# Kernel optimization log

Hardware: AMD Instinct MI355X
Metric: run time of the kernel (lower is better)

## Reference

```python
import jax, jax.numpy as jnp
import numpy as np

OMEGA_ENC = 0.01   # Encoder.omega
OMEGA_K = 0.1      # KernelMLP.omega
N0, E0 = 4096, 16384     # level-0 graph
N1, E1 = 1024, 8192      # level-1 (pooled) graph
F_IN, H, LAT, DIM = 8, 64, 32, 3
F = H + DIM              # conv input features (x || pos)


def _glorot(key, shape):
    s = jnp.sqrt(2.0 / (shape[0] + shape[-1]))
    return (jax.random.normal(key, shape) * s).astype(jnp.float32)


def setup_inputs() -> dict:
    key = jax.random.key(0)
    ks = jax.random.split(key, 24)
    inp = {
        "x": jax.random.normal(ks[0], (N0, F_IN), jnp.float32),
        "pos": jax.random.normal(ks[1], (N0, DIM), jnp.float32),
        "edge_index": jax.random.randint(ks[2], (2, E0), 0, N0),
        "pool_edge_index1": jax.random.randint(ks[3], (2, E1), 0, N1),
        "pool_pos1": jax.random.normal(ks[4], (N1, DIM), jnp.float32),
        "pool_keep_idx0": jnp.sort(jax.random.randint(ks[5], (N1,), 0, N0)),
        "lin0_w": _glorot(ks[6], (F_IN, H)),
        "lin0_b": 0.01 * jax.random.normal(ks[7], (H,), jnp.float32),
        "lin1_w": _glorot(ks[8], (H, LAT)),
        "lin1_b": 0.01 * jax.random.normal(ks[9], (LAT,), jnp.float32),
    }
    k = 10
    for i in range(2):
        inp[f"conv{i}_k_w0"] = _glorot(ks[k], (DIM + 1, H))
        inp[f"conv{i}_k_b0"] = 0.01 * jax.random.normal(ks[k + 1], (H,), jnp.float32)
        inp[f"conv{i}_k_w1"] = _glorot(ks[k + 2], (H, H))
        inp[f"conv{i}_k_b1"] = 0.01 * jax.random.normal(ks[k + 3], (H,), jnp.float32)
        inp[f"conv{i}_k_w2"] = _glorot(ks[k + 4], (H, F))
        inp[f"conv{i}_k_b2"] = 0.01 * jax.random.normal(ks[k + 5], (F,), jnp.float32)
        inp[f"conv{i}_bias"] = jnp.zeros((H,), jnp.float32)  # zeros() init in torch
        k += 6
    return inp


def _with_self_loops(ei, n):
    # add_remaining_self_loops: input edges are assumed self-loop-free
    loops = jnp.arange(n, dtype=ei.dtype)
    return jnp.concatenate([ei, jnp.stack([loops, loops])], axis=1)


def _kernel_conv(xf, ei, pos, n, w0, b0, w1, b1, w2, b2, bias):
    src, dst = ei[0], ei[1]
    rel = pos[dst] - pos[src]                               # [E,3]
    zero = jnp.all(rel == 0.0, axis=1)                      # self loops -> rho=0, nan phi in torch
    rel_s = jnp.where(zero[:, None], 1.0, rel)              # safe values (avoid nan grads)
    rho = jnp.sqrt(jnp.sum(rel_s * rel_s, axis=1))
    theta = jnp.arctan2(rel_s[:, 1], rel_s[:, 0])
    phi = jnp.arcsin(jnp.clip(rel_s[:, 2] / rho, -1.0, 1.0))
    # torch sets theta/phi to 0 where phi is nan (rho==0); rho itself is 0 there
    rho = jnp.where(zero, 0.0, rho)
    theta = jnp.where(zero, 0.0, theta)
    phi = jnp.where(zero, 0.0, phi)
    feats = jnp.stack([rho, theta / jnp.pi, phi / jnp.pi], axis=1)   # [E,3]
    # KernelMLP lin0 on (feats || channel_id), evaluated for all out channels at once
    base = feats @ w0[:DIM] + b0                            # [E,H]
    ch = jnp.arange(H, dtype=xf.dtype)                      # out_channels == H
    h0 = jnp.sin(OMEGA_K * (base[None] + ch[:, None, None] * w0[DIM][None, None]))  # [C,E,H]
    h1 = jnp.sin(OMEGA_K * (jnp.einsum('ceh,hk->cek', h0, w1) + b1))                # [C,E,H]
    x_j = xf[src]                                           # [E,F]
    # msg[e,c] = (lin2(h1[c,e]) * x_j[e]).sum(); lin2 folded into the contraction
    msg = jnp.einsum('ceh,hf,ef->ec', h1, w2, x_j) + (x_j @ b2)[:, None]            # [E,C]
    return jax.ops.segment_sum(msg, dst, num_segments=n) + bias


def reference(x, edge_index, pos, pool_edge_index1, pool_pos1, pool_keep_idx0,
              lin0_w, lin0_b, lin1_w, lin1_b,
              conv0_k_w0, conv0_k_b0, conv0_k_w1, conv0_k_b1, conv0_k_w2, conv0_k_b2, conv0_bias,
              conv1_k_w0, conv1_k_b0, conv1_k_w1, conv1_k_b1, conv1_k_w2, conv1_k_b2, conv1_bias):
    n0 = x.shape[0]
    h = jnp.sin(OMEGA_ENC * (x @ lin0_w + lin0_b))
    ei0 = _with_self_loops(edge_index, n0)
    h = jnp.sin(OMEGA_ENC * _kernel_conv(jnp.concatenate([h, pos], 1), ei0, pos, n0,
                                         conv0_k_w0, conv0_k_b0, conv0_k_w1, conv0_k_b1,
                                         conv0_k_w2, conv0_k_b2, conv0_bias))
    # max_pool_neighbor_x: per-node max over neighbors incl. self (self loops in ei0)
    h = jax.ops.segment_max(h[ei0[0]], ei0[1], num_segments=n0)[pool_keep_idx0]
    n1 = pool_pos1.shape[0]
    ei1 = _with_self_loops(pool_edge_index1, n1)
    h = jnp.sin(OMEGA_ENC * _kernel_conv(jnp.concatenate([h, pool_pos1], 1), ei1, pool_pos1, n1,
                                         conv1_k_w0, conv1_k_b0, conv1_k_w1, conv1_k_b1,
                                         conv1_k_w2, conv1_k_b2, conv1_bias))
    return jnp.sin(OMEGA_ENC * (h @ lin1_w + lin1_b))   # [N1, LAT]
```

## Files before the change

### kernel.cpp

```cpp
#include <hip/hip_runtime.h>
#include <hip/hip_fp16.h>

#define N0C 4096
#define E0C 16384
#define N1C 1024
#define E1C 8192
#define HC 64
#define FINC 8
#define LATC 32
#define FC 67
#define E0T (E0C + N0C)
#define E1T (E1C + N1C)

typedef float f32x4 __attribute__((ext_vector_type(4)));
typedef _Float16 f16x8 __attribute__((ext_vector_type(8)));

__global__ __launch_bounds__(256) void k_prep(
    const float* __restrict__ x, const float* __restrict__ l0w,
    const float* __restrict__ l0b, const float* __restrict__ posp,
    const float* __restrict__ c0w2, const float* __restrict__ c0b2,
    const float* __restrict__ c0w0, const float* __restrict__ c1w0,
    const float* __restrict__ c0w1, const float* __restrict__ c1w1,
    const int* __restrict__ ei0, const int* __restrict__ ei1,
    _Float16* __restrict__ bC0, _Float16* __restrict__ bS0,
    _Float16* __restrict__ bC1, _Float16* __restrict__ bS1,
    _Float16* __restrict__ w1f0, _Float16* __restrict__ w1f1,
    int* __restrict__ cnt, float* __restrict__ tN, float* __restrict__ dN) {
  if (blockIdx.x < 256) {
    __shared__ float w2s[64][69];
    __shared__ float xr[4][64];
    const int tid = threadIdx.x;
    const int wave = __builtin_amdgcn_readfirstlane(tid >> 6), lane = tid & 63;
    for (int idx = tid; idx < HC * FC; idx += 256)
      w2s[idx / FC][idx % FC] = c0w2[idx];
    __syncthreads();
#pragma unroll
    for (int i = 0; i < 4; ++i) {
      const int n = (blockIdx.x * 4 + wave) + i * 1024;
      float a = l0b[lane];
#pragma unroll
      for (int f = 0; f < FINC; ++f) a = fmaf(x[n * FINC + f], l0w[f * HC + lane], a);
      xr[wave][lane] = sinf(0.01f * a);
      __builtin_amdgcn_wave_barrier();
      const float px = posp[n * 3], py = posp[n * 3 + 1], pz = posp[n * 3 + 2];
      float tl = 0.f, ds = 0.f;
#pragma unroll 8
      for (int f = 0; f < HC; ++f) {
        float xv = xr[wave][f];
        tl = fmaf(xv, w2s[lane][f], tl);
        ds = fmaf(xv, c0b2[f], ds);
      }
      tl = fmaf(px, w2s[lane][64], fmaf(py, w2s[lane][65], fmaf(pz, w2s[lane][66], tl)));
      ds = fmaf(px, c0b2[64], fmaf(py, c0b2[65], fmaf(pz, c0b2[66], ds)));
      tN[n * HC + lane] = tl;
      if (lane == 0) dN[n] = ds;
      __builtin_amdgcn_wave_barrier();
    }
  } else {
    int id = (blockIdx.x - 256) * 256 + threadIdx.x;
    if (id < 8192) {
      int lvl = id >> 12, r = id & 4095;
      int fi = r >> 9, lane = (r >> 3) & 63, j = r & 7;
      int nt = fi & 3, ks = fi >> 2;
      int c = nt * 16 + (lane & 15);
      int h = ks * 32 + (lane >> 4) * 8 + j;
      const float* w = lvl ? c1w0 : c0w0;
      float s, cv;
      sincosf(0.1f * (float)c * w[3 * HC + h], &s, &cv);
      (lvl ? bC1 : bC0)[r] = (_Float16)cv;
      (lvl ? bS1 : bS0)[r] = (_Float16)s;
    } else if (id < 16384) {
      int r0 = id - 8192;
      int lvl = r0 >> 12, r = r0 & 4095;
      int fi = r >> 9, lane = (r >> 3) & 63, j = r & 7;
      int ms = fi & 3, ks = fi >> 2;
      int h = ks * 32 + (lane >> 4) * 8 + j;
      int kout = ms * 16 + (lane & 15);
      const float* w = lvl ? c1w1 : c0w1;
      (lvl ? w1f1 : w1f0)[r] = (_Float16)(0.1f * w[h * HC + kout]);
    } else if (id < 16384 + E0T + E1T) {
      int r = id - 16384;
      if (r < E0T) {
        int dst = (r < E0C) ? ei0[E0C + r] : (r - E0C);
        atomicAdd(cnt + dst, 1);
      } else {
        int e = r - E0T;
        int dst = (e < E1C) ? ei1[E1C + e] : (e - E1C);
        atomicAdd(cnt + N0C + dst, 1);
      }
    }
  }
}

__global__ void k_scan(const int* __restrict__ cnt, int* __restrict__ rp0,
                       int* __restrict__ rp1) {
  __shared__ int wsum[16];
  const int b = blockIdx.x;
  const int n = b ? N1C : N0C;
  const int* c = cnt + (b ? N0C : 0);
  int* rp = b ? rp1 : rp0;
  const int tid = threadIdx.x;
  const int lane = tid & 63, wid = tid >> 6;
  const int per = n >> 10;
  int loc[4];
  int sum = 0;
  for (int j = 0; j < per; ++j) { loc[j] = c[tid * per + j]; sum += loc[j]; }
  int xv = sum;
#pragma unroll
  for (int off = 1; off < 64; off <<= 1) {
    int v = __shfl_up(xv, off, 64);
    if (lane >= off) xv += v;
  }
  if (lane == 63) wsum[wid] = xv;
  __syncthreads();
  if (wid == 0) {
    int w = (lane < 16) ? wsum[lane] : 0;
#pragma unroll
    for (int off = 1; off < 16; off <<= 1) {
      int v = __shfl_up(w, off, 64);
      if (lane >= off) w += v;
    }
    if (lane < 16) wsum[lane] = w;
  }
  __syncthreads();
  int prefix = wid ? wsum[wid - 1] : 0;
  int incl = xv + prefix;
  int base = incl - sum;
  for (int j = 0; j < per; ++j) { rp[tid * per + j] = base; base += loc[j]; }
  if (tid == 1023) rp[n] = incl;
}

__global__ void k_scatter(const int* __restrict__ ei0, const int* __restrict__ ei1,
                          const int* __restrict__ rp0, const int* __restrict__ rp1,
                          int* __restrict__ fill, int* __restrict__ eidx0,
                          int* __restrict__ eidx1, int* __restrict__ inv0,
                          int* __restrict__ inv1) {
  int id = blockIdx.x * blockDim.x + threadIdx.x;
  if (id < E0T) {
    int dst = (id < E0C) ? ei0[E0C + id] : (id - E0C);
    int p = rp0[dst] + atomicAdd(fill + dst, 1);
    eidx0[p] = id;
    inv0[id] = p;
  } else if (id < E0T + E1T) {
    int e = id - E0T;
    int dst = (e < E1C) ? ei1[E1C + e] : (e - E1C);
    int p = rp1[dst] + atomicAdd(fill + N0C + dst, 1);
    eidx1[p] = e;
    inv1[e] = p;
  }
}

__global__ __launch_bounds__(256, 3) void k_conv(
    const int* __restrict__ ei, int E, int eTot,
    const float* __restrict__ posp,
    const float* __restrict__ tN, const float* __restrict__ dN,
    const float* __restrict__ kw0, const float* __restrict__ kb0,
    const _Float16* __restrict__ bC, const _Float16* __restrict__ bS,
    const _Float16* __restrict__ w1f, const float* __restrict__ b1,
    const int* __restrict__ inv, float* __restrict__ msg) {
  __shared__ __attribute__((aligned(16))) _Float16 bCs[4096], bSs[4096];
  __shared__ __attribute__((aligned(16))) _Float16 scS[4][2][64], scC[4][2][64];
  const int tid = threadIdx.x;
  const int wave = __builtin_amdgcn_readfirstlane(tid >> 6), lane = tid & 63;
  const int q = lane >> 4;
  for (int idx = tid; idx < 512; idx += 256) {
    ((f16x8*)bCs)[idx] = ((const f16x8*)bC)[idx];
    ((f16x8*)bSs)[idx] = ((const f16x8*)bS)[idx];
  }
  f16x8 w1r[8];
#pragma unroll
  for (int f = 0; f < 8; ++f) w1r[f] = *(const f16x8*)(w1f + ((f << 6) + lane) * 8);
  f32x4 bbq[4];
#pragma unroll
  for (int ms = 0; ms < 4; ++ms) {
    f32x4 t = *(const f32x4*)(b1 + ms * 16 + q * 4);
    bbq[ms] = t * 0.1f;
  }
  const float kb0v = kb0[lane];
  const float kw0x = kw0[lane], kw0y = kw0[HC + lane], kw0z = kw0[2 * HC + lane];
  __syncthreads();

  const int nW = gridDim.x * 4;
  int e = blockIdx.x * 4 + wave;
  if (e >= eTot) return;

  auto stg = [&](int ee, int& sN, float& sv, float& cv, float& dv) {
    int s, d2;
    if (ee < E) { s = ei[ee]; d2 = ei[E + ee]; } else { s = ee - E; d2 = s; }
    sN = s;
    const float px = posp[s * 3], py = posp[s * 3 + 1], pz = posp[s * 3 + 2];
    const float rx = posp[d2 * 3] - px;
    const float ry = posp[d2 * 3 + 1] - py;
    const float rz = posp[d2 * 3 + 2] - pz;
    float f0 = 0.f, f1 = 0.f, f2 = 0.f;
    if (!(rx == 0.f && ry == 0.f && rz == 0.f)) {
      const float PI_F = 3.14159265358979323846f;
      float rho = sqrtf(rx * rx + ry * ry + rz * rz);
      float th = atan2f(ry, rx);
      float ratio = fminf(1.f, fmaxf(-1.f, rz / rho));
      float ph = asinf(ratio);
      f0 = rho; f1 = th / PI_F; f2 = ph / PI_F;
    }
    float base = fmaf(f0, kw0x, fmaf(f1, kw0y, fmaf(f2, kw0z, kb0v)));
    sincosf(0.1f * base, &sv, &cv);
    dv = dN[s];
  };

  int s0;
  float sv0, cv0, dv0;
  stg(e, s0, sv0, cv0, dv0);
  int buf = 0;
  scS[wave][0][lane] = (_Float16)sv0;
  scC[wave][0][lane] = (_Float16)cv0;
  __builtin_amdgcn_wave_barrier();

  while (true) {
    const int en = e + nW;
    const bool more = en < eTot;
    f32x4 tr[4];
    {
      const float* trp = tN + (size_t)s0 * HC;
#pragma unroll
      for (int ms = 0; ms < 4; ++ms) tr[ms] = *(const f32x4*)(trp + ms * 16 + q * 4);
    }
    const int ip = inv[e];
    int s1 = 0;
    float sv1 = 0.f, cv1 = 0.f, dv1 = 0.f;
    if (more) {
      stg(en, s1, sv1, cv1, dv1);
      scS[wave][buf ^ 1][lane] = (_Float16)sv1;
      scC[wave][buf ^ 1][lane] = (_Float16)cv1;
    }
    __builtin_amdgcn_wave_barrier();

    f32x4 acc[4][4];
#pragma unroll
    for (int ms = 0; ms < 4; ++ms)
#pragma unroll
      for (int nt = 0; nt < 4; ++nt) acc[ms][nt] = bbq[ms];
#pragma unroll
    for (int ks = 0; ks < 2; ++ks) {
      f16x8 sv8 = *(const f16x8*)&scS[wave][buf][ks * 32 + q * 8];
      f16x8 cv8 = *(const f16x8*)&scC[wave][buf][ks * 32 + q * 8];
      f16x8 bf[4];
#pragma unroll
      for (int nt = 0; nt < 4; ++nt) {
        f16x8 cb = *(const f16x8*)&bCs[((ks * 4 + nt) * 64 + lane) * 8];
        f16x8 sb = *(const f16x8*)&bSs[((ks * 4 + nt) * 64 + lane) * 8];
        bf[nt] = sv8 * cb + cv8 * sb;
      }
#pragma unroll
      for (int ms = 0; ms < 4; ++ms)
#pragma unroll
        for (int nt = 0; nt < 4; ++nt)
          acc[ms][nt] = __builtin_amdgcn_mfma_f32_16x16x32_f16(
              w1r[ks * 4 + ms], bf[nt], acc[ms][nt], 0, 0, 0);
    }

    float snt0 = 0.f, snt1 = 0.f, snt2 = 0.f, snt3 = 0.f;
#pragma unroll
    for (int ms = 0; ms < 4; ++ms) {
#pragma unroll
      for (int r = 0; r < 4; ++r) {
        float tt = tr[ms][r];
        snt0 = fmaf(__sinf(acc[ms][0][r]), tt, snt0);
        snt1 = fmaf(__sinf(acc[ms][1][r]), tt, snt1);
        snt2 = fmaf(__sinf(acc[ms][2][r]), tt, snt2);
        snt3 = fmaf(__sinf(acc[ms][3][r]), tt, snt3);
      }
    }
    snt0 += __shfl_xor(snt0, 16, 64); snt0 += __shfl_xor(snt0, 32, 64);
    snt1 += __shfl_xor(snt1, 16, 64); snt1 += __shfl_xor(snt1, 32, 64);
    snt2 += __shfl_xor(snt2, 16, 64); snt2 += __shfl_xor(snt2, 32, 64);
    snt3 += __shfl_xor(snt3, 16, 64); snt3 += __shfl_xor(snt3, 32, 64);
    float val = (q == 0) ? snt0 : (q == 1) ? snt1 : (q == 2) ? snt2 : snt3;
    msg[(size_t)ip * HC + lane] = val + dv0;

    if (!more) break;
    e = en; s0 = s1; dv0 = dv1; buf ^= 1;
  }
}

__global__ void k_reduce0(const float* __restrict__ msg, const int* __restrict__ rp,
                          const float* __restrict__ bias, float* __restrict__ hc) {
  const int wave = threadIdx.x >> 6, lane = threadIdx.x & 63;
  const int n = blockIdx.x * 4 + wave;
  const int j0 = rp[n], j1 = rp[n + 1];
  const float* p = msg + (size_t)j0 * HC + lane;
  const int m = j1 - j0;
  float a0 = 0.f, a1 = 0.f;
  int j = 0;
  for (; j + 1 < m; j += 2) {
    a0 += p[(size_t)j * HC];
    a1 += p[(size_t)(j + 1) * HC];
  }
  if (j < m) a0 += p[(size_t)j * HC];
  hc[(size_t)n * HC + lane] = sinf(0.01f * (a0 + a1 + bias[lane]));
}

__global__ void k_pool1(const float* __restrict__ hc0, const int* __restrict__ eidx,
                        const int* __restrict__ rp, const int* __restrict__ ei,
                        const int* __restrict__ keep, const float* __restrict__ ppos,
                        const float* __restrict__ c1w2, const float* __restrict__ c1b2,
                        float* __restrict__ tN, float* __restrict__ dN) {
  __shared__ float w2s[64][69];
  __shared__ float xr[4][64];
  const int tid = threadIdx.x;
  const int wave = __builtin_amdgcn_readfirstlane(tid >> 6), lane = tid & 63;
  for (int idx = tid; idx < HC * FC; idx += 256)
    w2s[idx / FC][idx % FC] = c1w2[idx];
  const int i = blockIdx.x * 4 + wave;
  int n = keep[i];
  int j0 = rp[n], j1 = rp[n + 1];
  float m = -INFINITY;
  for (int j = j0; j < j1; ++j) {
    int e = eidx[j];
    int src = (e < E0C) ? ei[e] : (e - E0C);
    m = fmaxf(m, hc0[(size_t)src * HC + lane]);
  }
  xr[wave][lane] = m;
  __syncthreads();
  const float px = ppos[i * 3], py = ppos[i * 3 + 1], pz = ppos[i * 3 + 2];
  float tl = 0.f, ds = 0.f;
#pragma unroll 8
  for (int f = 0; f < HC; ++f) {
    float xv = xr[wave][f];
    tl = fmaf(xv, w2s[lane][f], tl);
    ds = fmaf(xv, c1b2[f], ds);
  }
  tl = fmaf(px, w2s[lane][64], fmaf(py, w2s[lane][65], fmaf(pz, w2s[lane][66], tl)));
  ds = fmaf(px, c1b2[64], fmaf(py, c1b2[65], fmaf(pz, c1b2[66], ds)));
  tN[i * HC + lane] = tl;
  if (lane == 0) dN[i] = ds;
}

__global__ void k_reduce1f(const float* __restrict__ msg, const int* __restrict__ rp,
                           const float* __restrict__ bias, const float* __restrict__ l1w,
                           const float* __restrict__ l1b, float* __restrict__ outp) {
  __shared__ float hr[4][64];
  const int wave = threadIdx.x >> 6, lane = threadIdx.x & 63;
  const int node = blockIdx.x * 4 + wave;
  const int j0 = rp[node], j1 = rp[node + 1];
  const float* p = msg + (size_t)j0 * HC + lane;
  const int m = j1 - j0;
  float a0 = 0.f, a1 = 0.f;
  int j = 0;
  for (; j + 1 < m; j += 2) {
    a0 += p[(size_t)j * HC];
    a1 += p[(size_t)(j + 1) * HC];
  }
  if (j < m) a0 += p[(size_t)j * HC];
  hr[wave][lane] = sinf(0.01f * (a0 + a1 + bias[lane]));
  __syncthreads();
  if (lane < LATC) {
    const float* h = hr[wave];
    float o = l1b[lane];
#pragma unroll 8
    for (int c = 0; c < HC; ++c) o = fmaf(h[c], l1w[c * LATC + lane], o);
    outp[node * LATC + lane] = sinf(0.01f * o);
  }
}

extern "C" void kernel_launch(void* const* d_in, const int* in_sizes, int n_in,
                              void* d_out, int out_size, void* d_ws, size_t ws_size,
                              hipStream_t stream) {
  (void)in_sizes; (void)n_in; (void)out_size; (void)ws_size;
  const float* x    = (const float*)d_in[0];
  const float* pos  = (const float*)d_in[1];
  const int*   ei   = (const int*)d_in[2];
  const int*   pei  = (const int*)d_in[3];
  const float* ppos = (const float*)d_in[4];
  const int*   keep = (const int*)d_in[5];
  const float* l0w  = (const float*)d_in[6];
  const float* l0b  = (const float*)d_in[7];
  const float* l1w  = (const float*)d_in[8];
  const float* l1b  = (const float*)d_in[9];
  const float* c0w0 = (const float*)d_in[10];
  const float* c0b0 = (const float*)d_in[11];
  const float* c0w1 = (const float*)d_in[12];
  const float* c0b1 = (const float*)d_in[13];
  const float* c0w2 = (const float*)d_in[14];
  const float* c0b2 = (const float*)d_in[15];
  const float* c0bias = (const float*)d_in[16];
  const float* c1w0 = (const float*)d_in[17];
  const float* c1b0 = (const float*)d_in[18];
  const float* c1w1 = (const float*)d_in[19];
  const float* c1b1 = (const float*)d_in[20];
  const float* c1w2 = (const float*)d_in[21];
  const float* c1b2 = (const float*)d_in[22];
  const float* c1bias = (const float*)d_in[23];
  float* outp = (float*)d_out;

  char* p = (char*)d_ws;
  auto carve = [&](size_t bytes) -> char* {
    char* r = p;
    p += (bytes + 255) & ~(size_t)255;
    return r;
  };
  float* hc0  = (float*)carve((size_t)N0C * HC * 4);
  float* tN0  = (float*)carve((size_t)N0C * HC * 4);
  float* dN0  = (float*)carve((size_t)N0C * 4);
  float* tN1  = (float*)carve((size_t)N1C * HC * 4);
  float* dN1  = (float*)carve((size_t)N1C * 4);
  _Float16* bC0  = (_Float16*)carve(4096 * 2);
  _Float16* bS0  = (_Float16*)carve(4096 * 2);
  _Float16* bC1  = (_Float16*)carve(4096 * 2);
  _Float16* bS1  = (_Float16*)carve(4096 * 2);
  _Float16* w1f0 = (_Float16*)carve(4096 * 2);
  _Float16* w1f1 = (_Float16*)carve(4096 * 2);
  int* cnt  = (int*)carve((size_t)(N0C + N1C) * 4);
  int* fill = (int*)carve((size_t)(N0C + N1C) * 4);
  int* rp0 = (int*)carve((size_t)(N0C + 1) * 4);
  int* rp1 = (int*)carve((size_t)(N1C + 1) * 4);
  int* eidx0 = (int*)carve((size_t)E0T * 4);
  int* eidx1 = (int*)carve((size_t)E1T * 4);
  int* inv0  = (int*)carve((size_t)E0T * 4);
  int* inv1  = (int*)carve((size_t)E1T * 4);
  float* msg = (float*)carve((size_t)E0T * HC * 4);

  hipMemsetAsync(cnt, 0, (size_t)(N0C + N1C) * 4 * 2, stream);

  k_prep<<<256 + 180, 256, 0, stream>>>(x, l0w, l0b, pos, c0w2, c0b2,
                                        c0w0, c1w0, c0w1, c1w1, ei, pei,
                                        bC0, bS0, bC1, bS1, w1f0, w1f1,
                                        cnt, tN0, dN0);
  k_scan<<<2, 1024, 0, stream>>>(cnt, rp0, rp1);
  k_scatter<<<(E0T + E1T + 255) / 256, 256, 0, stream>>>(ei, pei, rp0, rp1, fill,
                                                         eidx0, eidx1, inv0, inv1);
  k_conv<<<1536, 256, 0, stream>>>(ei, E0C, E0T, pos, tN0, dN0, c0w0, c0b0,
                                   bC0, bS0, w1f0, c0b1, inv0, msg);
  k_reduce0<<<N0C / 4, 256, 0, stream>>>(msg, rp0, c0bias, hc0);
  k_pool1<<<N1C / 4, 256, 0, stream>>>(hc0, eidx0, rp0, ei, keep, ppos,
                                       c1w2, c1b2, tN1, dN1);
  k_conv<<<768, 256, 0, stream>>>(pei, E1C, E1T, ppos, tN1, dN1, c1w0, c1b0,
                                  bC1, bS1, w1f1, c1b1, inv1, msg);
  k_reduce1f<<<N1C / 4, 256, 0, stream>>>(msg, rp1, c1bias, l1w, l1b, outp);
}
```

Measured before the change: 181.4 us.

## Replace CSR build and per-node reductions with atomic scatter-add and atomic max pooling

```diff
diff --git a/kernel.cpp b/kernel.cpp
--- a/kernel.cpp
+++ b/kernel.cpp
@@ -21,11 +21,10 @@
     const float* __restrict__ c0w2, const float* __restrict__ c0b2,
     const float* __restrict__ c0w0, const float* __restrict__ c1w0,
     const float* __restrict__ c0w1, const float* __restrict__ c1w1,
-    const int* __restrict__ ei0, const int* __restrict__ ei1,
     _Float16* __restrict__ bC0, _Float16* __restrict__ bS0,
     _Float16* __restrict__ bC1, _Float16* __restrict__ bS1,
     _Float16* __restrict__ w1f0, _Float16* __restrict__ w1f1,
-    int* __restrict__ cnt, float* __restrict__ tN, float* __restrict__ dN) {
+    float* __restrict__ tN, float* __restrict__ dN) {
   if (blockIdx.x < 256) {
     __shared__ float w2s[64][69];
     __shared__ float xr[4][64];
@@ -69,7 +68,7 @@
       sincosf(0.1f * (float)c * w[3 * HC + h], &s, &cv);
       (lvl ? bC1 : bC0)[r] = (_Float16)cv;
       (lvl ? bS1 : bS0)[r] = (_Float16)s;
-    } else if (id < 16384) {
+    } else {
       int r0 = id - 8192;
       int lvl = r0 >> 12, r = r0 & 4095;
       int fi = r >> 9, lane = (r >> 3) & 63, j = r & 7;
@@ -78,75 +77,7 @@
       int kout = ms * 16 + (lane & 15);
       const float* w = lvl ? c1w1 : c0w1;
       (lvl ? w1f1 : w1f0)[r] = (_Float16)(0.1f * w[h * HC + kout]);
-    } else if (id < 16384 + E0T + E1T) {
-      int r = id - 16384;
-      if (r < E0T) {
-        int dst = (r < E0C) ? ei0[E0C + r] : (r - E0C);
-        atomicAdd(cnt + dst, 1);
-      } else {
-        int e = r - E0T;
-        int dst = (e < E1C) ? ei1[E1C + e] : (e - E1C);
-        atomicAdd(cnt + N0C + dst, 1);
-      }
-    }
-  }
-}
-
-__global__ void k_scan(const int* __restrict__ cnt, int* __restrict__ rp0,
-                       int* __restrict__ rp1) {
-  __shared__ int wsum[16];
-  const int b = blockIdx.x;
-  const int n = b ? N1C : N0C;
-  const int* c = cnt + (b ? N0C : 0);
-  int* rp = b ? rp1 : rp0;
-  const int tid = threadIdx.x;
-  const int lane = tid & 63, wid = tid >> 6;
-  const int per = n >> 10;
-  int loc[4];
-  int sum = 0;
-  for (int j = 0; j < per; ++j) { loc[j] = c[tid * per + j]; sum += loc[j]; }
-  int xv = sum;
-#pragma unroll
-  for (int off = 1; off < 64; off <<= 1) {
-    int v = __shfl_up(xv, off, 64);
-    if (lane >= off) xv += v;
-  }
-  if (lane == 63) wsum[wid] = xv;
-  __syncthreads();
-  if (wid == 0) {
-    int w = (lane < 16) ? wsum[lane] : 0;
-#pragma unroll
-    for (int off = 1; off < 16; off <<= 1) {
-      int v = __shfl_up(w, off, 64);
-      if (lane >= off) w += v;
-    }
-    if (lane < 16) wsum[lane] = w;
-  }
-  __syncthreads();
-  int prefix = wid ? wsum[wid - 1] : 0;
-  int incl = xv + prefix;
-  int base = incl - sum;
-  for (int j = 0; j < per; ++j) { rp[tid * per + j] = base; base += loc[j]; }
-  if (tid == 1023) rp[n] = incl;
-}
-
-__global__ void k_scatter(const int* __restrict__ ei0, const int* __restrict__ ei1,
-                          const int* __restrict__ rp0, const int* __restrict__ rp1,
-                          int* __restrict__ fill, int* __restrict__ eidx0,
-                          int* __restrict__ eidx1, int* __restrict__ inv0,
-                          int* __restrict__ inv1) {
-  int id = blockIdx.x * blockDim.x + threadIdx.x;
-  if (id < E0T) {
-    int dst = (id < E0C) ? ei0[E0C + id] : (id - E0C);
-    int p = rp0[dst] + atomicAdd(fill + dst, 1);
-    eidx0[p] = id;
-    inv0[id] = p;
-  } else if (id < E0T + E1T) {
-    int e = id - E0T;
-    int dst = (e < E1C) ? ei1[E1C + e] : (e - E1C);
-    int p = rp1[dst] + atomicAdd(fill + N0C + dst, 1);
-    eidx1[p] = e;
-    inv1[e] = p;
+    }
   }
 }
 
@@ -157,7 +88,7 @@
     const float* __restrict__ kw0, const float* __restrict__ kb0,
     const _Float16* __restrict__ bC, const _Float16* __restrict__ bS,
     const _Float16* __restrict__ w1f, const float* __restrict__ b1,
-    const int* __restrict__ inv, float* __restrict__ msg) {
+    float* __restrict__ acc_out) {
   __shared__ __attribute__((aligned(16))) _Float16 bCs[4096], bSs[4096];
   __shared__ __attribute__((aligned(16))) _Float16 scS[4][2][64], scC[4][2][64];
   const int tid = threadIdx.x;
@@ -184,10 +115,11 @@
   int e = blockIdx.x * 4 + wave;
   if (e >= eTot) return;
 
-  auto stg = [&](int ee, int& sN, float& sv, float& cv, float& dv) {
+  auto stg = [&](int ee, int& sN, int& dTo, float& sv, float& cv, float& dv) {
     int s, d2;
     if (ee < E) { s = ei[ee]; d2 = ei[E + ee]; } else { s = ee - E; d2 = s; }
     sN = s;
+    dTo = d2;
     const float px = posp[s * 3], py = posp[s * 3 + 1], pz = posp[s * 3 + 2];
     const float rx = posp[d2 * 3] - px;
     const float ry = posp[d2 * 3 + 1] - py;
@@ -202,13 +134,13 @@
       f0 = rho; f1 = th / PI_F; f2 = ph / PI_F;
     }
     float base = fmaf(f0, kw0x, fmaf(f1, kw0y, fmaf(f2, kw0z, kb0v)));
-    sincosf(0.1f * base, &sv, &cv);
+    __sincosf(0.1f * base, &sv, &cv);
     dv = dN[s];
   };
 
-  int s0;
+  int s0, d0;
   float sv0, cv0, dv0;
-  stg(e, s0, sv0, cv0, dv0);
+  stg(e, s0, d0, sv0, cv0, dv0);
   int buf = 0;
   scS[wave][0][lane] = (_Float16)sv0;
   scC[wave][0][lane] = (_Float16)cv0;
@@ -223,11 +155,10 @@
 #pragma unroll
       for (int ms = 0; ms < 4; ++ms) tr[ms] = *(const f32x4*)(trp + ms * 16 + q * 4);
     }
-    const int ip = inv[e];
-    int s1 = 0;
+    int s1 = 0, d1 = 0;
     float sv1 = 0.f, cv1 = 0.f, dv1 = 0.f;
     if (more) {
-      stg(en, s1, sv1, cv1, dv1);
+      stg(en, s1, d1, sv1, cv1, dv1);
       scS[wave][buf ^ 1][lane] = (_Float16)sv1;
       scC[wave][buf ^ 1][lane] = (_Float16)cv1;
     }
@@ -274,35 +205,30 @@
     snt2 += __shfl_xor(snt2, 16, 64); snt2 += __shfl_xor(snt2, 32, 64);
     snt3 += __shfl_xor(snt3, 16, 64); snt3 += __shfl_xor(snt3, 32, 64);
     float val = (q == 0) ? snt0 : (q == 1) ? snt1 : (q == 2) ? snt2 : snt3;
-    msg[(size_t)ip * HC + lane] = val + dv0;
+    atomicAdd(acc_out + (size_t)d0 * HC + lane, val + dv0);
 
     if (!more) break;
-    e = en; s0 = s1; dv0 = dv1; buf ^= 1;
-  }
-}
-
-__global__ void k_reduce0(const float* __restrict__ msg, const int* __restrict__ rp,
-                          const float* __restrict__ bias, float* __restrict__ hc) {
+    e = en; s0 = s1; d0 = d1; dv0 = dv1; buf ^= 1;
+  }
+}
+
+__global__ __launch_bounds__(256) void k_pool(
+    const int* __restrict__ ei, const float* __restrict__ acc0,
+    const float* __restrict__ bias, unsigned int* __restrict__ pooled) {
   const int wave = threadIdx.x >> 6, lane = threadIdx.x & 63;
-  const int n = blockIdx.x * 4 + wave;
-  const int j0 = rp[n], j1 = rp[n + 1];
-  const float* p = msg + (size_t)j0 * HC + lane;
-  const int m = j1 - j0;
-  float a0 = 0.f, a1 = 0.f;
-  int j = 0;
-  for (; j + 1 < m; j += 2) {
-    a0 += p[(size_t)j * HC];
-    a1 += p[(size_t)(j + 1) * HC];
-  }
-  if (j < m) a0 += p[(size_t)j * HC];
-  hc[(size_t)n * HC + lane] = sinf(0.01f * (a0 + a1 + bias[lane]));
-}
-
-__global__ void k_pool1(const float* __restrict__ hc0, const int* __restrict__ eidx,
-                        const int* __restrict__ rp, const int* __restrict__ ei,
-                        const int* __restrict__ keep, const float* __restrict__ ppos,
-                        const float* __restrict__ c1w2, const float* __restrict__ c1b2,
-                        float* __restrict__ tN, float* __restrict__ dN) {
+  const int e = blockIdx.x * 4 + wave;
+  int s, d;
+  if (e < E0C) { s = ei[e]; d = ei[E0C + e]; } else { s = e - E0C; d = s; }
+  float v = sinf(0.01f * (acc0[(size_t)s * HC + lane] + bias[lane]));
+  unsigned int b = __float_as_uint(v);
+  unsigned int key = (b & 0x80000000u) ? ~b : (b | 0x80000000u);
+  atomicMax(pooled + (size_t)d * HC + lane, key);
+}
+
+__global__ __launch_bounds__(256) void k_t1(
+    const unsigned int* __restrict__ pooled, const int* __restrict__ keep,
+    const float* __restrict__ ppos, const float* __restrict__ c1w2,
+    const float* __restrict__ c1b2, float* __restrict__ tN, float* __restrict__ dN) {
   __shared__ float w2s[64][69];
   __shared__ float xr[4][64];
   const int tid = threadIdx.x;
@@ -310,15 +236,10 @@
   for (int idx = tid; idx < HC * FC; idx += 256)
     w2s[idx / FC][idx % FC] = c1w2[idx];
   const int i = blockIdx.x * 4 + wave;
-  int n = keep[i];
-  int j0 = rp[n], j1 = rp[n + 1];
-  float m = -INFINITY;
-  for (int j = j0; j < j1; ++j) {
-    int e = eidx[j];
-    int src = (e < E0C) ? ei[e] : (e - E0C);
-    m = fmaxf(m, hc0[(size_t)src * HC + lane]);
-  }
-  xr[wave][lane] = m;
+  const int n = keep[i];
+  unsigned int key = pooled[(size_t)n * HC + lane];
+  unsigned int b = (key & 0x80000000u) ? (key & 0x7FFFFFFFu) : ~key;
+  xr[wave][lane] = __uint_as_float(b);
   __syncthreads();
   const float px = ppos[i * 3], py = ppos[i * 3 + 1], pz = ppos[i * 3 + 2];
   float tl = 0.f, ds = 0.f;
@@ -334,23 +255,14 @@
   if (lane == 0) dN[i] = ds;
 }
 
-__global__ void k_reduce1f(const float* __restrict__ msg, const int* __restrict__ rp,
-                           const float* __restrict__ bias, const float* __restrict__ l1w,
-                           const float* __restrict__ l1b, float* __restrict__ outp) {
+__global__ __launch_bounds__(256) void k_final(
+    const float* __restrict__ acc1, const float* __restrict__ bias,
+    const float* __restrict__ l1w, const float* __restrict__ l1b,
+    float* __restrict__ outp) {
   __shared__ float hr[4][64];
   const int wave = threadIdx.x >> 6, lane = threadIdx.x & 63;
   const int node = blockIdx.x * 4 + wave;
-  const int j0 = rp[node], j1 = rp[node + 1];
-  const float* p = msg + (size_t)j0 * HC + lane;
-  const int m = j1 - j0;
-  float a0 = 0.f, a1 = 0.f;
-  int j = 0;
-  for (; j + 1 < m; j += 2) {
-    a0 += p[(size_t)j * HC];
-    a1 += p[(size_t)(j + 1) * HC];
-  }
-  if (j < m) a0 += p[(size_t)j * HC];
-  hr[wave][lane] = sinf(0.01f * (a0 + a1 + bias[lane]));
+  hr[wave][lane] = sinf(0.01f * (acc1[(size_t)node * HC + lane] + bias[lane]));
   __syncthreads();
   if (lane < LATC) {
     const float* h = hr[wave];
@@ -397,7 +309,6 @@
     p += (bytes + 255) & ~(size_t)255;
     return r;
   };
-  float* hc0  = (float*)carve((size_t)N0C * HC * 4);
   float* tN0  = (float*)carve((size_t)N0C * HC * 4);
   float* dN0  = (float*)carve((size_t)N0C * 4);
   float* tN1  = (float*)carve((size_t)N1C * HC * 4);
@@ -408,31 +319,21 @@
   _Float16* bS1  = (_Float16*)carve(4096 * 2);
   _Float16* w1f0 = (_Float16*)carve(4096 * 2);
   _Float16* w1f1 = (_Float16*)carve(4096 * 2);
-  int* cnt  = (int*)carve((size_t)(N0C + N1C) * 4);
-  int* fill = (int*)carve((size_t)(N0C + N1C) * 4);
-  int* rp0 = (int*)carve((size_t)(N0C + 1) * 4);
-  int* rp1 = (int*)carve((size_t)(N1C + 1) * 4);
-  int* eidx0 = (int*)carve((size_t)E0T * 4);
-  int* eidx1 = (int*)carve((size_t)E1T * 4);
-  int* inv0  = (int*)carve((size_t)E0T * 4);
-  int* inv1  = (int*)carve((size_t)E1T * 4);
-  float* msg = (float*)carve((size_t)E0T * HC * 4);
-
-  hipMemsetAsync(cnt, 0, (size_t)(N0C + N1C) * 4 * 2, stream);
-
-  k_prep<<<256 + 180, 256, 0, stream>>>(x, l0w, l0b, pos, c0w2, c0b2,
-                                        c0w0, c1w0, c0w1, c1w1, ei, pei,
-                                        bC0, bS0, bC1, bS1, w1f0, w1f1,
-                                        cnt, tN0, dN0);
-  k_scan<<<2, 1024, 0, stream>>>(cnt, rp0, rp1);
-  k_scatter<<<(E0T + E1T + 255) / 256, 256, 0, stream>>>(ei, pei, rp0, rp1, fill,
-                                                         eidx0, eidx1, inv0, inv1);
+  float* acc0 = (float*)carve((size_t)N0C * HC * 4);
+  unsigned int* pooled = (unsigned int*)carve((size_t)N0C * HC * 4);
+  float* acc1 = (float*)carve((size_t)N1C * HC * 4);
+
+  hipMemsetAsync(acc0, 0, (size_t)(N0C + N0C + N1C) * HC * 4, stream);
+
+  k_prep<<<256 + 64, 256, 0, stream>>>(x, l0w, l0b, pos, c0w2, c0b2,
+                                       c0w0, c1w0, c0w1, c1w1,
+                                       bC0, bS0, bC1, bS1, w1f0, w1f1,
+                                       tN0, dN0);
   k_conv<<<1536, 256, 0, stream>>>(ei, E0C, E0T, pos, tN0, dN0, c0w0, c0b0,
-                                   bC0, bS0, w1f0, c0b1, inv0, msg);
-  k_reduce0<<<N0C / 4, 256, 0, stream>>>(msg, rp0, c0bias, hc0);
-  k_pool1<<<N1C / 4, 256, 0, stream>>>(hc0, eidx0, rp0, ei, keep, ppos,
-                                       c1w2, c1b2, tN1, dN1);
+                                   bC0, bS0, w1f0, c0b1, acc0);
+  k_pool<<<E0T / 4, 256, 0, stream>>>(ei, acc0, c0bias, pooled);
+  k_t1<<<N1C / 4, 256, 0, stream>>>(pooled, keep, ppos, c1w2, c1b2, tN1, dN1);
   k_conv<<<768, 256, 0, stream>>>(pei, E1C, E1T, ppos, tN1, dN1, c1w0, c1b0,
-                                  bC1, bS1, w1f1, c1b1, inv1, msg);
-  k_reduce1f<<<N1C / 4, 256, 0, stream>>>(msg, rp1, c1bias, l1w, l1b, outp);
-}
+                                  bC1, bS1, w1f1, c1b1, acc1);
+  k_final<<<N1C / 4, 256, 0, stream>>>(acc1, c1bias, l1w, l1b, outp);
+}
```

Result: faster. 167.2 us (-7.9%).
